# Optimization experiments

Hardware: AMD Instinct MI355X
Metric: run time of the kernel (lower is better)

Reference implementation:

```python
import jax, jax.numpy as jnp
import numpy as np

NUM_HEADS = 8
GN_GROUPS = 32
GN_EPS = 1e-5


def group_norm(x, gamma, beta):
    b, c, h, w = x.shape
    xg = x.reshape(b, GN_GROUPS, c // GN_GROUPS, h, w)
    mean = xg.mean(axis=(2, 3, 4), keepdims=True)
    var = xg.var(axis=(2, 3, 4), keepdims=True)
    xn = ((xg - mean) * jax.lax.rsqrt(var + GN_EPS)).reshape(b, c, h, w)
    return xn * gamma[None, :, None, None] + beta[None, :, None, None]


def setup_inputs() -> dict:
    key = jax.random.key(0)
    ks = jax.random.split(key, 3)
    c = 512
    x = jax.random.normal(ks[0], (8, c, 32, 32), dtype=jnp.float32)
    gn_gamma = jnp.ones((c,), jnp.float32)
    gn_beta = jnp.zeros((c,), jnp.float32)
    # 1x1 conv weights stored as [out_ch, in_ch]; scaled for numerical sanity
    w_qkv = jax.random.normal(ks[1], (3 * c, c), dtype=jnp.float32) * 0.02
    b_qkv = jnp.zeros((3 * c,), jnp.float32)
    w_out = jax.random.normal(ks[2], (c, c), dtype=jnp.float32) * 0.02
    b_out = jnp.zeros((c,), jnp.float32)
    return {"x": x, "gn_gamma": gn_gamma, "gn_beta": gn_beta,
            "w_qkv": w_qkv, "b_qkv": b_qkv, "w_out": w_out, "b_out": b_out}


def reference(x, gn_gamma, gn_beta, w_qkv, b_qkv, w_out, b_out):
    b, c, h, w = x.shape
    hd = c // NUM_HEADS
    scale = 1.0 / jnp.sqrt(jnp.float32(hd))
    residual = x
    xn = group_norm(x, gn_gamma, gn_beta)
    # 1x1 conv == channel matmul: [b, 3c, h, w]
    qkv = jnp.einsum('oc,bchw->bohw', w_qkv, xn) + b_qkv[None, :, None, None]
    q, k, v = jnp.split(qkv, 3, axis=1)
    hw = h * w
    q = q.reshape(b * NUM_HEADS, hd, hw)
    k = k.reshape(b * NUM_HEADS, hd, hw)
    v = v.reshape(b * NUM_HEADS, hd, hw)
    scores = jnp.einsum('ndi,ndj->nij', q, k) * scale  # [b*nh, hw, hw]
    probs = jax.nn.softmax(scores, axis=-1)
    out = jnp.einsum('nij,ndj->nid', probs, v)          # [b*nh, hw, hd]
    out = out.transpose(0, 2, 1).reshape(b, c, h, w)
    out = jnp.einsum('oc,bchw->bohw', w_out, out) + b_out[None, :, None, None]
    return out + residual
```

## Files before the change

kernel.cpp:

```cpp
#include <hip/hip_runtime.h>
#include <math.h>

#define NHEADS 8
#define C 512
#define HW 1024
#define HD 64

typedef __bf16 bf16x8 __attribute__((ext_vector_type(8)));
typedef __bf16 bf16x4 __attribute__((ext_vector_type(4)));
typedef float f32x4 __attribute__((ext_vector_type(4)));

__global__ __launch_bounds__(256) void wcvt_kernel(const float* __restrict__ w1,
                                                   __bf16* __restrict__ o1,
                                                   const float* __restrict__ w2,
                                                   __bf16* __restrict__ o2) {
  int id = blockIdx.x * 2048 + threadIdx.x * 8;
  const float* src;
  __bf16* dst;
  int off;
  if (id < 786432) { src = w1; dst = o1; off = id; }
  else { src = w2; dst = o2; off = id - 786432; }
  float4 a = *(const float4*)(src + off);
  float4 b = *(const float4*)(src + off + 4);
  bf16x8 o;
  o[0] = (__bf16)a.x; o[1] = (__bf16)a.y; o[2] = (__bf16)a.z; o[3] = (__bf16)a.w;
  o[4] = (__bf16)b.x; o[5] = (__bf16)b.y; o[6] = (__bf16)b.z; o[7] = (__bf16)b.w;
  *(bf16x8*)(dst + off) = o;
}

__global__ __launch_bounds__(256) void gn_kernel(const float* __restrict__ x,
                                                 const float* __restrict__ gamma,
                                                 const float* __restrict__ beta,
                                                 __bf16* __restrict__ xnT) {
  int b = blockIdx.x >> 5, g = blockIdx.x & 31;
  const size_t base = ((size_t)b * C + (size_t)g * 16) * HW;
  const float4* xp = (const float4*)(x + base);
  int tid = threadIdx.x;

  float s = 0.f, ss = 0.f;
  float4 v[16];
#pragma unroll
  for (int it = 0; it < 16; it++) {
    v[it] = xp[tid + it * 256];
    s += v[it].x + v[it].y + v[it].z + v[it].w;
    ss += v[it].x * v[it].x + v[it].y * v[it].y + v[it].z * v[it].z + v[it].w * v[it].w;
  }
#pragma unroll
  for (int off = 32; off > 0; off >>= 1) {
    s += __shfl_down(s, off);
    ss += __shfl_down(ss, off);
  }
  __shared__ float red[8];
  __shared__ float mi[2];
  int wid = tid >> 6;
  if ((tid & 63) == 0) { red[wid] = s; red[4 + wid] = ss; }
  __syncthreads();
  if (tid == 0) {
    float S = red[0] + red[1] + red[2] + red[3];
    float SS = red[4] + red[5] + red[6] + red[7];
    float mean = S * (1.f / 16384.f);
    float var = SS * (1.f / 16384.f) - mean * mean;
    mi[0] = mean;
    mi[1] = rsqrtf(var + 1e-5f);
  }
  __syncthreads();
  float mean = mi[0], inv = mi[1];
  float ga[16], be[16];
#pragma unroll
  for (int it = 0; it < 16; it++) {
    float g_ = gamma[g * 16 + it] * inv;
    ga[it] = g_;
    be[it] = beta[g * 16 + it] - mean * g_;
  }
  __bf16* dstb = xnT + ((size_t)b * HW + (size_t)tid * 4) * C + g * 16;
#pragma unroll
  for (int jj = 0; jj < 4; jj++) {
    bf16x8 w0, w1;
#pragma unroll
    for (int e = 0; e < 8; e++) {
      w0[e] = (__bf16)(((const float*)&v[e])[jj] * ga[e] + be[e]);
      w1[e] = (__bf16)(((const float*)&v[e + 8])[jj] * ga[e + 8] + be[e + 8]);
    }
    *(bf16x8*)(dstb + (size_t)jj * C) = w0;
    *(bf16x8*)(dstb + (size_t)jj * C + 8) = w1;
  }
}

template <int EPI>
__global__ __launch_bounds__(256) void gemm_rr(const __bf16* __restrict__ Rp, size_t Rbs,
                                               const __bf16* __restrict__ Cp, size_t Cbs,
                                               const float* __restrict__ bias,
                                               __bf16* __restrict__ q_or_v,
                                               __bf16* __restrict__ kT,
                                               const float* __restrict__ resid,
                                               float* __restrict__ Yout) {
  int bx = blockIdx.x, by = blockIdx.y, b = blockIdx.z;
  int tid = threadIdx.x, wid = tid >> 6, lane = tid & 63;
  int l15 = lane & 15, lhi = lane >> 4;
  int wr = wid >> 1, wc = wid & 1;

  const __bf16* Rb = Rp + (size_t)b * Rbs + (size_t)by * 128 * 512;
  const __bf16* Cb = Cp + (size_t)b * Cbs + (size_t)bx * 128 * 512;

  __shared__ __align__(16) char smem[32768];
  char* Rs = smem;
  char* Cs = smem + 16384;

  f32x4 acc[4][4] = {};
  int srow = tid >> 1, sc0 = (tid & 1) * 4;

  for (int kk = 0; kk < 512; kk += 64) {
    __syncthreads();
    const __bf16* rg = Rb + (size_t)srow * 512 + kk + sc0 * 8;
    const __bf16* cg = Cb + (size_t)srow * 512 + kk + sc0 * 8;
#pragma unroll
    for (int q = 0; q < 4; q++) {
      int c = sc0 + q;
      int o = srow * 128 + ((c ^ (srow & 7)) << 4);
      *(uint4*)(Rs + o) = *(const uint4*)(rg + q * 8);
      *(uint4*)(Cs + o) = *(const uint4*)(cg + q * 8);
    }
    __syncthreads();
#pragma unroll
    for (int ks = 0; ks < 2; ks++) {
      bf16x8 ar[4], br[4];
      int c = ks * 4 + lhi;
#pragma unroll
      for (int m = 0; m < 4; m++) {
        int row = wr * 64 + m * 16 + l15;
        ar[m] = *(const bf16x8*)(Rs + row * 128 + ((c ^ (row & 7)) << 4));
      }
#pragma unroll
      for (int n = 0; n < 4; n++) {
        int row = wc * 64 + n * 16 + l15;
        br[n] = *(const bf16x8*)(Cs + row * 128 + ((c ^ (row & 7)) << 4));
      }
#pragma unroll
      for (int m = 0; m < 4; m++)
#pragma unroll
        for (int n = 0; n < 4; n++)
          acc[m][n] = __builtin_amdgcn_mfma_f32_16x16x32_bf16(ar[m], br[n], acc[m][n], 0, 0, 0);
    }
  }

  int rbase = by * 128 + wr * 64;
  int cbase = bx * 128 + wc * 64;

  if (EPI == 0) {
#pragma unroll
    for (int n = 0; n < 4; n++) {
      int col = cbase + n * 16 + l15;
      int sec = col >> 9;
      int h = (col >> 6) & 7;
      int d = col & 63;
      __bf16* dst0 = (sec ? kT : q_or_v) + ((size_t)b * 8 + h) * (size_t)(HW * HD) + d;
      float bs = bias[col];
#pragma unroll
      for (int m = 0; m < 4; m++)
#pragma unroll
        for (int r = 0; r < 4; r++) {
          int i = rbase + m * 16 + lhi * 4 + r;
          dst0[(size_t)i * HD] = (__bf16)(acc[m][n][r] + bs);
        }
    }
  } else if (EPI == 1) {
#pragma unroll
    for (int m = 0; m < 4; m++)
#pragma unroll
      for (int r = 0; r < 4; r++) {
        int row = rbase + m * 16 + lhi * 4 + r;
        int h = row >> 6, d = row & 63;
        float bs = bias[row];
        __bf16* dst = q_or_v + (((size_t)b * 8 + h) * HD + d) * HW;
#pragma unroll
        for (int n = 0; n < 4; n++) {
          int j = cbase + n * 16 + l15;
          dst[j] = (__bf16)(acc[m][n][r] + bs);
        }
      }
  } else {
#pragma unroll
    for (int m = 0; m < 4; m++)
#pragma unroll
      for (int r = 0; r < 4; r++) {
        int o = rbase + m * 16 + lhi * 4 + r;
        float bs = bias[o];
        size_t base2 = ((size_t)b * C + o) * HW;
#pragma unroll
        for (int n = 0; n < 4; n++) {
          int j = cbase + n * 16 + l15;
          Yout[base2 + j] = acc[m][n][r] + bs + resid[base2 + j];
        }
      }
  }
}

__global__ __launch_bounds__(256) void attn_mfma_kernel(const __bf16* __restrict__ qT,
                                                        const __bf16* __restrict__ kT,
                                                        const __bf16* __restrict__ vN,
                                                        __bf16* __restrict__ aT) {
  int qt = blockIdx.x;
  int bh = blockIdx.y;
  int tid = threadIdx.x;
  int wid = tid >> 6;
  int lane = tid & 63;
  int l15 = lane & 15;
  int lhi = lane >> 4;

  const __bf16* qh = qT + (size_t)bh * HW * HD;
  const __bf16* kh = kT + (size_t)bh * HW * HD;
  const __bf16* vh = vN + (size_t)bh * HD * HW;

  __shared__ __align__(16) char smem[32768];
  char* kt = smem;
  char* vt = smem + 8192;
  char* pb = smem + 16384 + wid * 4096;

  int i0 = qt * 128 + wid * 32;

  bf16x8 qf[2][2];
#pragma unroll
  for (int it = 0; it < 2; it++)
#pragma unroll
    for (int ks = 0; ks < 2; ks++) {
      int row = i0 + it * 16 + l15;
      qf[it][ks] = *(const bf16x8*)(qh + (size_t)row * HD + ks * 32 + lhi * 8);
    }

  f32x4 accO[2][4] = {};
  float m[2][4], l[2][4];
#pragma unroll
  for (int it = 0; it < 2; it++)
#pragma unroll
    for (int r = 0; r < 4; r++) { m[it][r] = -1e30f; l[it][r] = 0.f; }

  for (int t = 0; t < 16; ++t) {
    int j0 = t * 64;
    __syncthreads();
#pragma unroll
    for (int s = 0; s < 2; ++s) {
      int L = tid + s * 256;
      int r = L >> 3, c = L & 7;
      uint4 kd = *(const uint4*)((const char*)kh + (size_t)(j0 + r) * 128 + c * 16);
      uint4 vd = *(const uint4*)((const char*)vh + (size_t)r * 2048 + j0 * 2 + c * 16);
      *(uint4*)(kt + r * 128 + ((c ^ (r & 7)) << 4)) = kd;
      *(uint4*)(vt + r * 128 + ((c ^ (r & 7)) << 4)) = vd;
    }
    __syncthreads();

    f32x4 s_[2][4] = {};
#pragma unroll
    for (int ks = 0; ks < 2; ++ks)
#pragma unroll
      for (int jt = 0; jt < 4; ++jt) {
        int j = jt * 16 + l15;
        int c = ks * 4 + lhi;
        bf16x8 bk = *(const bf16x8*)(kt + j * 128 + ((c ^ (j & 7)) << 4));
        s_[0][jt] = __builtin_amdgcn_mfma_f32_16x16x32_bf16(qf[0][ks], bk, s_[0][jt], 0, 0, 0);
        s_[1][jt] = __builtin_amdgcn_mfma_f32_16x16x32_bf16(qf[1][ks], bk, s_[1][jt], 0, 0, 0);
      }

#pragma unroll
    for (int it = 0; it < 2; ++it) {
      float pm[4];
#pragma unroll
      for (int r = 0; r < 4; r++) {
        pm[r] = -1e30f;
#pragma unroll
        for (int jt = 0; jt < 4; ++jt) {
          s_[it][jt][r] *= 0.125f;
          pm[r] = fmaxf(pm[r], s_[it][jt][r]);
        }
      }
#pragma unroll
      for (int off = 1; off < 16; off <<= 1)
#pragma unroll
        for (int r = 0; r < 4; r++) pm[r] = fmaxf(pm[r], __shfl_xor(pm[r], off));
      float corr[4];
#pragma unroll
      for (int r = 0; r < 4; r++) {
        float nm = fmaxf(m[it][r], pm[r]);
        corr[r] = __expf(m[it][r] - nm);
        m[it][r] = nm;
      }
      float rsum[4] = {0.f, 0.f, 0.f, 0.f};
#pragma unroll
      for (int jt = 0; jt < 4; ++jt)
#pragma unroll
        for (int r = 0; r < 4; r++) {
          float p = __expf(s_[it][jt][r] - m[it][r]);
          s_[it][jt][r] = p;
          rsum[r] += p;
        }
#pragma unroll
      for (int off = 1; off < 16; off <<= 1)
#pragma unroll
        for (int r = 0; r < 4; r++) rsum[r] += __shfl_xor(rsum[r], off);
#pragma unroll
      for (int r = 0; r < 4; r++) l[it][r] = l[it][r] * corr[r] + rsum[r];
#pragma unroll
      for (int dt = 0; dt < 4; ++dt)
#pragma unroll
        for (int r = 0; r < 4; r++) accO[it][dt][r] *= corr[r];
#pragma unroll
      for (int jt = 0; jt < 4; ++jt)
#pragma unroll
        for (int r = 0; r < 4; r++) {
          int row = it * 16 + lhi * 4 + r;
          int j = jt * 16 + l15;
          int off2 = row * 128 + (((j >> 3) ^ (row & 7)) << 4) + (j & 7) * 2;
          *(__bf16*)(pb + off2) = (__bf16)s_[it][jt][r];
        }
    }

#pragma unroll
    for (int kj = 0; kj < 2; ++kj) {
      bf16x8 pa[2];
#pragma unroll
      for (int it = 0; it < 2; ++it) {
        int row = it * 16 + l15;
        int c = kj * 4 + lhi;
        pa[it] = *(const bf16x8*)(pb + row * 128 + ((c ^ (row & 7)) << 4));
      }
#pragma unroll
      for (int dt = 0; dt < 4; ++dt) {
        int d = dt * 16 + l15;
        int c = kj * 4 + lhi;
        bf16x8 bv = *(const bf16x8*)(vt + d * 128 + ((c ^ (d & 7)) << 4));
        accO[0][dt] = __builtin_amdgcn_mfma_f32_16x16x32_bf16(pa[0], bv, accO[0][dt], 0, 0, 0);
        accO[1][dt] = __builtin_amdgcn_mfma_f32_16x16x32_bf16(pa[1], bv, accO[1][dt], 0, 0, 0);
      }
    }
  }

  __syncthreads();
  __bf16* Lo = (__bf16*)(smem + wid * 4608);
#pragma unroll
  for (int it = 0; it < 2; ++it)
#pragma unroll
    for (int r = 0; r < 4; r++) {
      float inv = 1.f / l[it][r];
      int iloc = it * 16 + lhi * 4 + r;
#pragma unroll
      for (int dt = 0; dt < 4; ++dt)
        Lo[iloc * 72 + dt * 16 + l15] = (__bf16)(accO[it][dt][r] * inv);
    }
  __syncthreads();
  int b = bh >> 3, hh = bh & 7;
  int iloc = lane >> 1, dh = (lane & 1) * 32;
  __bf16* dst = aT + ((size_t)b * HW + i0 + iloc) * C + hh * 64 + dh;
  const __bf16* srcl = Lo + iloc * 72 + dh;
#pragma unroll
  for (int s2 = 0; s2 < 4; s2++)
    *(uint4*)(dst + s2 * 8) = *(const uint4*)(srcl + s2 * 8);
}

extern "C" void kernel_launch(void* const* d_in, const int* in_sizes, int n_in,
                              void* d_out, int out_size, void* d_ws, size_t ws_size,
                              hipStream_t stream) {
  const float* x = (const float*)d_in[0];
  const float* gamma = (const float*)d_in[1];
  const float* beta = (const float*)d_in[2];
  const float* w_qkv = (const float*)d_in[3];
  const float* b_qkv = (const float*)d_in[4];
  const float* w_out = (const float*)d_in[5];
  const float* b_out = (const float*)d_in[6];
  float* out = (float*)d_out;

  char* ws = (char*)d_ws;
  const size_t MB = 1024 * 1024;
  __bf16* xnT = (__bf16*)ws;
  __bf16* qT  = (__bf16*)(ws + 8 * MB);
  __bf16* kT  = (__bf16*)(ws + 16 * MB);
  __bf16* vN  = (__bf16*)(ws + 24 * MB);
  __bf16* aT  = (__bf16*)(ws + 32 * MB);
  __bf16* wbq = (__bf16*)(ws + 40 * MB);
  __bf16* wbo = (__bf16*)(ws + 42 * MB);

  wcvt_kernel<<<dim3(512), 256, 0, stream>>>(w_qkv, wbq, w_out, wbo);
  gn_kernel<<<dim3(256), 256, 0, stream>>>(x, gamma, beta, xnT);
  gemm_rr<0><<<dim3(8, 8, 8), 256, 0, stream>>>(xnT, (size_t)HW * C, wbq, 0,
                                                b_qkv, qT, kT, nullptr, nullptr);
  gemm_rr<1><<<dim3(8, 4, 8), 256, 0, stream>>>(wbq + (size_t)1024 * 512, 0, xnT, (size_t)HW * C,
                                                b_qkv + 1024, vN, nullptr, nullptr, nullptr);
  attn_mfma_kernel<<<dim3(8, 64), 256, 0, stream>>>(qT, kT, vN, aT);
  gemm_rr<2><<<dim3(8, 4, 8), 256, 0, stream>>>(wbo, 0, aT, (size_t)HW * C,
                                                b_out, nullptr, nullptr, x, out);
}
```

Measured before the change: 193.5 us.

## Double-buffer K/V tiles, lazy softmax rescale, MFMA row sums in attention

The attention kernel now prefetches the next K/V tile into registers and writes it to a second shared-memory buffer after the PV MFMAs, leaving one barrier per iteration instead of two. The softmax scale is folded into Q at load time, and the running max is only updated (with its shuffles and accumulator rescale) when some row's tile max exceeds the old max by more than 8. Row sums come from an MFMA against a ones vector instead of shuffle reductions, and the grid is flattened so blocks of the same head spread across workgroups. Shared memory grows to 48KB, which may lower occupancy, and pre-rounding Q to bf16 after scaling slightly changes numerics.

```diff
diff --git a/kernel.cpp b/kernel.cpp
--- a/kernel.cpp
+++ b/kernel.cpp
@@ -199,8 +199,8 @@
                                                         const __bf16* __restrict__ kT,
                                                         const __bf16* __restrict__ vN,
                                                         __bf16* __restrict__ aT) {
-  int qt = blockIdx.x;
-  int bh = blockIdx.y;
+  int bh = blockIdx.x & 63;
+  int qt = blockIdx.x >> 6;
   int tid = threadIdx.x;
   int wid = tid >> 6;
   int lane = tid & 63;
@@ -208,13 +208,11 @@
   int lhi = lane >> 4;
 
   const __bf16* qh = qT + (size_t)bh * HW * HD;
-  const __bf16* kh = kT + (size_t)bh * HW * HD;
-  const __bf16* vh = vN + (size_t)bh * HD * HW;
-
-  __shared__ __align__(16) char smem[32768];
-  char* kt = smem;
-  char* vt = smem + 8192;
-  char* pb = smem + 16384 + wid * 4096;
+  const char* kh = (const char*)(kT + (size_t)bh * HW * HD);
+  const char* vh = (const char*)(vN + (size_t)bh * HD * HW);
+
+  __shared__ __align__(16) char smem[49152];
+  char* pb = smem + 32768 + wid * 4096;
 
   int i0 = qt * 128 + wid * 32;
 
@@ -224,29 +222,52 @@
 #pragma unroll
     for (int ks = 0; ks < 2; ks++) {
       int row = i0 + it * 16 + l15;
-      qf[it][ks] = *(const bf16x8*)(qh + (size_t)row * HD + ks * 32 + lhi * 8);
-    }
+      bf16x8 qv = *(const bf16x8*)(qh + (size_t)row * HD + ks * 32 + lhi * 8);
+#pragma unroll
+      for (int e = 0; e < 8; e++) qv[e] = (__bf16)((float)qv[e] * 0.125f);
+      qf[it][ks] = qv;
+    }
+
+  int sr = tid >> 3, sc = tid & 7;
+  int sr2 = sr + 32;
+  int swz1 = sr * 128 + ((sc ^ (sr & 7)) << 4);
+  int swz2 = sr2 * 128 + ((sc ^ (sr2 & 7)) << 4);
+
+  uint4 kr0, kr1, vr0, vr1;
+  {
+    kr0 = *(const uint4*)(kh + (size_t)sr * 128 + sc * 16);
+    kr1 = *(const uint4*)(kh + (size_t)sr2 * 128 + sc * 16);
+    vr0 = *(const uint4*)(vh + (size_t)sr * 2048 + sc * 16);
+    vr1 = *(const uint4*)(vh + (size_t)sr2 * 2048 + sc * 16);
+    *(uint4*)(smem + swz1) = kr0;
+    *(uint4*)(smem + swz2) = kr1;
+    *(uint4*)(smem + 8192 + swz1) = vr0;
+    *(uint4*)(smem + 8192 + swz2) = vr1;
+  }
 
   f32x4 accO[2][4] = {};
-  float m[2][4], l[2][4];
+  f32x4 lacc[2] = {};
+  float m[2][4];
 #pragma unroll
   for (int it = 0; it < 2; it++)
 #pragma unroll
-    for (int r = 0; r < 4; r++) { m[it][r] = -1e30f; l[it][r] = 0.f; }
+    for (int r = 0; r < 4; r++) m[it][r] = -1e30f;
+
+  bf16x8 ones;
+#pragma unroll
+  for (int e = 0; e < 8; e++) ones[e] = (__bf16)1.0f;
 
   for (int t = 0; t < 16; ++t) {
-    int j0 = t * 64;
+    if (t < 15) {
+      int j0n = (t + 1) * 64;
+      kr0 = *(const uint4*)(kh + (size_t)(j0n + sr) * 128 + sc * 16);
+      kr1 = *(const uint4*)(kh + (size_t)(j0n + sr2) * 128 + sc * 16);
+      vr0 = *(const uint4*)(vh + (size_t)sr * 2048 + j0n * 2 + sc * 16);
+      vr1 = *(const uint4*)(vh + (size_t)sr2 * 2048 + j0n * 2 + sc * 16);
+    }
     __syncthreads();
-#pragma unroll
-    for (int s = 0; s < 2; ++s) {
-      int L = tid + s * 256;
-      int r = L >> 3, c = L & 7;
-      uint4 kd = *(const uint4*)((const char*)kh + (size_t)(j0 + r) * 128 + c * 16);
-      uint4 vd = *(const uint4*)((const char*)vh + (size_t)r * 2048 + j0 * 2 + c * 16);
-      *(uint4*)(kt + r * 128 + ((c ^ (r & 7)) << 4)) = kd;
-      *(uint4*)(vt + r * 128 + ((c ^ (r & 7)) << 4)) = vd;
-    }
-    __syncthreads();
+    const char* kt = smem + ((t & 1) << 14);
+    const char* vt = kt + 8192;
 
     f32x4 s_[2][4] = {};
 #pragma unroll
@@ -260,58 +281,49 @@
         s_[1][jt] = __builtin_amdgcn_mfma_f32_16x16x32_bf16(qf[1][ks], bk, s_[1][jt], 0, 0, 0);
       }
 
-#pragma unroll
-    for (int it = 0; it < 2; ++it) {
-      float pm[4];
+    float lm[2][4];
+    int ok = 1;
+#pragma unroll
+    for (int it = 0; it < 2; ++it)
 #pragma unroll
       for (int r = 0; r < 4; r++) {
-        pm[r] = -1e30f;
-#pragma unroll
-        for (int jt = 0; jt < 4; ++jt) {
-          s_[it][jt][r] *= 0.125f;
-          pm[r] = fmaxf(pm[r], s_[it][jt][r]);
+        lm[it][r] = fmaxf(fmaxf(s_[it][0][r], s_[it][1][r]),
+                          fmaxf(s_[it][2][r], s_[it][3][r]));
+        ok &= (lm[it][r] <= m[it][r] + 8.f);
+      }
+    if (!__all(ok)) {
+#pragma unroll
+      for (int it = 0; it < 2; ++it) {
+        float pm[4];
+#pragma unroll
+        for (int r = 0; r < 4; r++) pm[r] = lm[it][r];
+#pragma unroll
+        for (int off = 1; off < 16; off <<= 1)
+#pragma unroll
+          for (int r = 0; r < 4; r++) pm[r] = fmaxf(pm[r], __shfl_xor(pm[r], off));
+#pragma unroll
+        for (int r = 0; r < 4; r++) {
+          float nm = fmaxf(m[it][r], pm[r]);
+          float corr = __expf(m[it][r] - nm);
+          m[it][r] = nm;
+          lacc[it][r] *= corr;
+#pragma unroll
+          for (int dt = 0; dt < 4; ++dt) accO[it][dt][r] *= corr;
         }
       }
-#pragma unroll
-      for (int off = 1; off < 16; off <<= 1)
-#pragma unroll
-        for (int r = 0; r < 4; r++) pm[r] = fmaxf(pm[r], __shfl_xor(pm[r], off));
-      float corr[4];
-#pragma unroll
-      for (int r = 0; r < 4; r++) {
-        float nm = fmaxf(m[it][r], pm[r]);
-        corr[r] = __expf(m[it][r] - nm);
-        m[it][r] = nm;
-      }
-      float rsum[4] = {0.f, 0.f, 0.f, 0.f};
+    }
+#pragma unroll
+    for (int it = 0; it < 2; ++it)
 #pragma unroll
       for (int jt = 0; jt < 4; ++jt)
 #pragma unroll
         for (int r = 0; r < 4; r++) {
           float p = __expf(s_[it][jt][r] - m[it][r]);
-          s_[it][jt][r] = p;
-          rsum[r] += p;
-        }
-#pragma unroll
-      for (int off = 1; off < 16; off <<= 1)
-#pragma unroll
-        for (int r = 0; r < 4; r++) rsum[r] += __shfl_xor(rsum[r], off);
-#pragma unroll
-      for (int r = 0; r < 4; r++) l[it][r] = l[it][r] * corr[r] + rsum[r];
-#pragma unroll
-      for (int dt = 0; dt < 4; ++dt)
-#pragma unroll
-        for (int r = 0; r < 4; r++) accO[it][dt][r] *= corr[r];
-#pragma unroll
-      for (int jt = 0; jt < 4; ++jt)
-#pragma unroll
-        for (int r = 0; r < 4; r++) {
           int row = it * 16 + lhi * 4 + r;
           int j = jt * 16 + l15;
           int off2 = row * 128 + (((j >> 3) ^ (row & 7)) << 4) + (j & 7) * 2;
-          *(__bf16*)(pb + off2) = (__bf16)s_[it][jt][r];
+          *(__bf16*)(pb + off2) = (__bf16)p;
         }
-    }
 
 #pragma unroll
     for (int kj = 0; kj < 2; ++kj) {
@@ -322,6 +334,8 @@
         int c = kj * 4 + lhi;
         pa[it] = *(const bf16x8*)(pb + row * 128 + ((c ^ (row & 7)) << 4));
       }
+      lacc[0] = __builtin_amdgcn_mfma_f32_16x16x32_bf16(pa[0], ones, lacc[0], 0, 0, 0);
+      lacc[1] = __builtin_amdgcn_mfma_f32_16x16x32_bf16(pa[1], ones, lacc[1], 0, 0, 0);
 #pragma unroll
       for (int dt = 0; dt < 4; ++dt) {
         int d = dt * 16 + l15;
@@ -331,6 +345,14 @@
         accO[1][dt] = __builtin_amdgcn_mfma_f32_16x16x32_bf16(pa[1], bv, accO[1][dt], 0, 0, 0);
       }
     }
+
+    if (t < 15) {
+      char* ktn = smem + (((t + 1) & 1) << 14);
+      *(uint4*)(ktn + swz1) = kr0;
+      *(uint4*)(ktn + swz2) = kr1;
+      *(uint4*)(ktn + 8192 + swz1) = vr0;
+      *(uint4*)(ktn + 8192 + swz2) = vr1;
+    }
   }
 
   __syncthreads();
@@ -339,7 +361,7 @@
   for (int it = 0; it < 2; ++it)
 #pragma unroll
     for (int r = 0; r < 4; r++) {
-      float inv = 1.f / l[it][r];
+      float inv = 1.f / lacc[it][r];
       int iloc = it * 16 + lhi * 4 + r;
 #pragma unroll
       for (int dt = 0; dt < 4; ++dt)
@@ -383,7 +405,7 @@
                                                 b_qkv, qT, kT, nullptr, nullptr);
   gemm_rr<1><<<dim3(8, 4, 8), 256, 0, stream>>>(wbq + (size_t)1024 * 512, 0, xnT, (size_t)HW * C,
                                                 b_qkv + 1024, vN, nullptr, nullptr, nullptr);
-  attn_mfma_kernel<<<dim3(8, 64), 256, 0, stream>>>(qT, kT, vN, aT);
+  attn_mfma_kernel<<<dim3(512), 256, 0, stream>>>(qT, kT, vN, aT);
   gemm_rr<2><<<dim3(8, 4, 8), 256, 0, stream>>>(wbo, 0, aT, (size_t)HW * C,
                                                 b_out, nullptr, nullptr, x, out);
 }
```

Result: faster. 173.2 us (-10.5%).
